# Performance work log

Hardware: AMD Instinct MI355X
Metric: run time of the kernel (lower is better)

## Reference

```python
import jax, jax.numpy as jnp
import numpy as np

EMBED_DIM = 512
NUM_HEADS = 16
WIN = (8, 8)
N_TOK = WIN[0] * WIN[1]           # 64 tokens per window
HEAD_DIM = EMBED_DIM // NUM_HEADS  # 32
SCALE = HEAD_DIM ** -0.5
B_WIN = 1024                       # batch * num_windows
NUM_WINDOWS = 256                  # windows per image -> batch images = 4


def _relative_bias_index(window_size):
    wh, ww = window_size
    coords = np.stack(np.meshgrid(np.arange(wh), np.arange(ww), indexing='ij'))  # (2, wh, ww)
    flat = coords.reshape(2, -1)                                   # (2, N)
    rel = (flat[:, :, None] - flat[:, None, :]).transpose(1, 2, 0)  # (N, N, 2)
    rel[:, :, 0] += wh - 1
    rel[:, :, 1] += ww - 1
    rel[:, :, 0] *= 2 * ww - 1
    return rel.sum(-1)  # (N, N) int


def setup_inputs() -> dict:
    key = jax.random.key(0)
    ks = jax.random.split(key, 6)
    x = jax.random.normal(ks[0], (B_WIN, N_TOK, EMBED_DIM), dtype=jnp.float32)
    attention_mask = jax.random.normal(ks[1], (NUM_WINDOWS, N_TOK, N_TOK), dtype=jnp.float32)
    qkv_w = jax.random.normal(ks[2], (EMBED_DIM, 3 * EMBED_DIM), dtype=jnp.float32) * 0.02
    qkv_b = jnp.zeros((3 * EMBED_DIM,), dtype=jnp.float32)
    proj_w = jax.random.normal(ks[3], (EMBED_DIM, EMBED_DIM), dtype=jnp.float32) * 0.02
    proj_b = jnp.zeros((EMBED_DIM,), dtype=jnp.float32)
    n_bias = (2 * WIN[0] - 1) * (2 * WIN[1] - 1)  # 225
    bias_table = jax.random.normal(ks[4], (n_bias, NUM_HEADS), dtype=jnp.float32) * 0.02
    rel_index = jnp.asarray(_relative_bias_index(WIN), dtype=jnp.int32)  # (N, N)
    return {"x": x, "attention_mask": attention_mask, "qkv_w": qkv_w, "qkv_b": qkv_b,
            "proj_w": proj_w, "proj_b": proj_b, "bias_table": bias_table, "rel_index": rel_index}


def reference(x, attention_mask, qkv_w, qkv_b, proj_w, proj_b, bias_table, rel_index):
    B, N, C = x.shape
    nw = attention_mask.shape[0]
    bimg = B // nw
    qkv = x @ qkv_w + qkv_b                              # (B, N, 3C)
    # original rearrange 'b n (h d c) -> d b n h c' groups last dim as (heads, 3, head_dim)
    qkv = qkv.reshape(B, N, NUM_HEADS, 3, HEAD_DIM)
    q, k, v = qkv[..., 0, :], qkv[..., 1, :], qkv[..., 2, :]  # each (B, N, H, hd)
    attn = jnp.einsum('bqhd,bkhd->bhqk', q, k) * SCALE        # (B, H, N, N)
    bias = bias_table[rel_index].transpose(2, 0, 1)           # (H, N, N)
    attn = attn + bias[None]
    attn = attn.reshape(bimg, nw, NUM_HEADS, N, N) + attention_mask[None, :, None]
    attn = jax.nn.softmax(attn, axis=-1).reshape(B, NUM_HEADS, N, N)
    out = jnp.einsum('bhqk,bkhd->bqhd', attn, v).reshape(B, N, C)
    return out @ proj_w + proj_b
```

## Files before the change

kernel.cpp:

```cpp
#include <hip/hip_runtime.h>
#include <hip/hip_bf16.h>


typedef unsigned short u16;
typedef __bf16 bx8 __attribute__((ext_vector_type(8)));
typedef float f4_t __attribute__((ext_vector_type(4)));

#define QKV_ELEMS 33554432ull
#define SCALE 0.17677669529663687f

static __device__ __forceinline__ u16 f2b(float f) {
    return __builtin_bit_cast(u16, (__bf16)f);
}

__global__ void wt_k(const float* __restrict__ W, u16* __restrict__ Wt,
                     int K, int N) {
    int idx = blockIdx.x * 256 + threadIdx.x;
    if (idx >= N * K) return;
    int n = idx / K, k = idx - n * K;
    Wt[idx] = f2b(W[(size_t)k * N + n]);
}

__global__ void bias_k(const float* __restrict__ bias_table,
                       const int* __restrict__ rel_index,
                       float* __restrict__ bias_full) {
    int idx = blockIdx.x * 256 + threadIdx.x;
    int h = idx >> 12, rc = idx & 4095;
    bias_full[idx] = bias_table[rel_index[rc] * 16 + h];
}

template <int MODE>
__global__ __launch_bounds__(256) void gemm_k(
    const void* __restrict__ Av, const u16* __restrict__ Bt,
    const float* __restrict__ bias, void* __restrict__ Out, int K) {
    const int tid  = threadIdx.x;
    const int wave = tid >> 6, lane = tid & 63;
    const int quad = lane >> 4, l16 = lane & 15;
    const int wm = wave >> 1, wn = wave & 1;
    const int m0 = blockIdx.y * 128, n0 = blockIdx.x * 128;
    const int N = gridDim.x * 128;

    __shared__ alignas(16) u16 a_s[128 * 40];
    __shared__ alignas(16) u16 b_s[128 * 40];

    f4_t acc[4][4];
#pragma unroll
    for (int i = 0; i < 4; ++i)
#pragma unroll
        for (int j = 0; j < 4; ++j) acc[i][j] = (f4_t){0.f, 0.f, 0.f, 0.f};

    for (int kt = 0; kt < K; kt += 32) {
        if (MODE == 0) {
            const float* A = (const float*)Av;
#pragma unroll
            for (int r = 0; r < 4; ++r) {
                int f = tid + 256 * r;
                int row = f >> 3, c4 = (f & 7) * 4;
                float4 v = *(const float4*)(A + (size_t)(m0 + row) * K + kt + c4);
                ushort4 p;
                p.x = f2b(v.x); p.y = f2b(v.y); p.z = f2b(v.z); p.w = f2b(v.w);
                *(ushort4*)&a_s[row * 40 + c4] = p;
            }
        } else {
            const u16* A = (const u16*)Av;
#pragma unroll
            for (int r = 0; r < 2; ++r) {
                int u = tid + 256 * r;
                int row = u >> 2, c8 = (u & 3) * 8;
                uint4 v = *(const uint4*)(A + (size_t)(m0 + row) * K + kt + c8);
                *(uint4*)&a_s[row * 40 + c8] = v;
            }
        }
#pragma unroll
        for (int r = 0; r < 2; ++r) {
            int u = tid + 256 * r;
            int row = u >> 2, c8 = (u & 3) * 8;
            uint4 v = *(const uint4*)(Bt + (size_t)(n0 + row) * K + kt + c8);
            *(uint4*)&b_s[row * 40 + c8] = v;
        }
        __syncthreads();

        bx8 af[4], bfr[4];
#pragma unroll
        for (int mt = 0; mt < 4; ++mt)
            af[mt] = *(const bx8*)&a_s[(wm * 64 + mt * 16 + l16) * 40 + quad * 8];
#pragma unroll
        for (int nt = 0; nt < 4; ++nt)
            bfr[nt] = *(const bx8*)&b_s[(wn * 64 + nt * 16 + l16) * 40 + quad * 8];
#pragma unroll
        for (int mt = 0; mt < 4; ++mt)
#pragma unroll
            for (int nt = 0; nt < 4; ++nt)
                acc[mt][nt] = __builtin_amdgcn_mfma_f32_16x16x32_bf16(
                    af[mt], bfr[nt], acc[mt][nt], 0, 0, 0);
        __syncthreads();
    }

    if (MODE == 0) {
        u16* qkv = (u16*)Out;
#pragma unroll
        for (int mt = 0; mt < 4; ++mt)
#pragma unroll
            for (int nt = 0; nt < 4; ++nt)
#pragma unroll
                for (int i = 0; i < 4; ++i) {
                    int r = m0 + wm * 64 + mt * 16 + quad * 4 + i;
                    int c = n0 + wn * 64 + nt * 16 + l16;
                    float v = acc[mt][nt][i] + bias[c];
                    int w = r >> 6, tok = r & 63;
                    int h = c / 96, rr = c - h * 96;
                    int which = rr >> 5, dd = rr & 31;
                    qkv[(size_t)which * QKV_ELEMS +
                        ((size_t)((w * 16 + h) * 64 + tok)) * 32 + dd] = f2b(v);
                }
    } else {
        float* Of = (float*)Out;
#pragma unroll
        for (int mt = 0; mt < 4; ++mt)
#pragma unroll
            for (int nt = 0; nt < 4; ++nt)
#pragma unroll
                for (int i = 0; i < 4; ++i) {
                    int r = m0 + wm * 64 + mt * 16 + quad * 4 + i;
                    int c = n0 + wn * 64 + nt * 16 + l16;
                    Of[(size_t)r * N + c] = acc[mt][nt][i] + bias[c];
                }
    }
}

__global__ __launch_bounds__(256) void attn_k(
    const u16* __restrict__ qkv, const float* __restrict__ mask,
    const float* __restrict__ biasf, u16* __restrict__ attn_out) {
    const int bx = blockIdx.x;
    const int w = bx >> 4, h = bx & 15;
    const int wmk = w & 255;
    const int tid = threadIdx.x;
    const int wave = tid >> 6, lane = tid & 63;
    const int quad = lane >> 4, l16 = lane & 15;

    __shared__ alignas(16) u16 q_s[64 * 40];
    __shared__ alignas(16) u16 k_s[64 * 40];
    __shared__ alignas(16) u16 vT[32 * 72];
    __shared__ float s_s[64 * 68];
    __shared__ alignas(16) u16 p_s[64 * 72];

    const size_t base = (size_t)((w << 4) + h) * 2048;
    {
        int tok = tid >> 2, d0 = (tid & 3) * 8;
        uint4 qv = *(const uint4*)(qkv + base + tid * 8);
        *(uint4*)&q_s[tok * 40 + d0] = qv;
        uint4 kv = *(const uint4*)(qkv + QKV_ELEMS + base + tid * 8);
        *(uint4*)&k_s[tok * 40 + d0] = kv;
        uint4 vv = *(const uint4*)(qkv + 2 * QKV_ELEMS + base + tid * 8);
        const u16* pv = (const u16*)&vv;
#pragma unroll
        for (int j = 0; j < 8; ++j) vT[(d0 + j) * 72 + tok] = pv[j];
    }
    __syncthreads();

    {
        bx8 a = *(const bx8*)&q_s[(wave * 16 + l16) * 40 + quad * 8];
#pragma unroll
        for (int nt = 0; nt < 4; ++nt) {
            bx8 b = *(const bx8*)&k_s[(nt * 16 + l16) * 40 + quad * 8];
            f4_t acc = (f4_t){0.f, 0.f, 0.f, 0.f};
            acc = __builtin_amdgcn_mfma_f32_16x16x32_bf16(a, b, acc, 0, 0, 0);
#pragma unroll
            for (int i = 0; i < 4; ++i) {
                int r = wave * 16 + quad * 4 + i;
                int c = nt * 16 + l16;
                float s = acc[i] * SCALE + biasf[(h << 12) + (r << 6) + c] +
                          mask[((size_t)wmk * 64 + r) * 64 + c];
                s_s[r * 68 + c] = s;
            }
        }
    }
    __syncthreads();

    {
        int row = tid >> 2, j = (tid & 3) * 16;
        float mx = -1e30f;
#pragma unroll
        for (int cc = 0; cc < 16; ++cc) mx = fmaxf(mx, s_s[row * 68 + j + cc]);
        mx = fmaxf(mx, __shfl_xor(mx, 1));
        mx = fmaxf(mx, __shfl_xor(mx, 2));
        float e[16], sum = 0.f;
#pragma unroll
        for (int cc = 0; cc < 16; ++cc) {
            e[cc] = __expf(s_s[row * 68 + j + cc] - mx);
            sum += e[cc];
        }
        sum += __shfl_xor(sum, 1);
        sum += __shfl_xor(sum, 2);
        float inv = 1.f / sum;
#pragma unroll
        for (int cc = 0; cc < 16; ++cc) p_s[row * 72 + j + cc] = f2b(e[cc] * inv);
    }
    __syncthreads();

    {
#pragma unroll
        for (int nt = 0; nt < 2; ++nt) {
            f4_t acc = (f4_t){0.f, 0.f, 0.f, 0.f};
#pragma unroll
            for (int ks = 0; ks < 2; ++ks) {
                bx8 a = *(const bx8*)&p_s[(wave * 16 + l16) * 72 + ks * 32 + quad * 8];
                bx8 b = *(const bx8*)&vT[(nt * 16 + l16) * 72 + ks * 32 + quad * 8];
                acc = __builtin_amdgcn_mfma_f32_16x16x32_bf16(a, b, acc, 0, 0, 0);
            }
#pragma unroll
            for (int i = 0; i < 4; ++i) {
                int r = wave * 16 + quad * 4 + i;
                int c = nt * 16 + l16;
                attn_out[((size_t)(w * 64 + r) << 9) + (h << 5) + c] = f2b(acc[i]);
            }
        }
    }
}

extern "C" void kernel_launch(void* const* d_in, const int* in_sizes, int n_in,
                              void* d_out, int out_size, void* d_ws,
                              size_t ws_size, hipStream_t stream) {
    const float* x      = (const float*)d_in[0];
    const float* mask   = (const float*)d_in[1];
    const float* qkv_w  = (const float*)d_in[2];
    const float* qkv_b  = (const float*)d_in[3];
    const float* proj_w = (const float*)d_in[4];
    const float* proj_b = (const float*)d_in[5];
    const float* bias_t = (const float*)d_in[6];
    const int*   rel    = (const int*)d_in[7];
    float* out = (float*)d_out;

    char* ws = (char*)d_ws;
    u16* Wt1 = (u16*)ws;      ws += (size_t)1536 * 512 * 2;
    u16* Wt2 = (u16*)ws;      ws += (size_t)512 * 512 * 2;
    float* biasf = (float*)ws; ws += (size_t)16 * 64 * 64 * 4;
    u16* qkv = (u16*)ws;      ws += 3 * QKV_ELEMS * 2;
    u16* attn = (u16*)ws;     ws += QKV_ELEMS * 2;

    wt_k<<<3072, 256, 0, stream>>>(qkv_w, Wt1, 512, 1536);
    wt_k<<<1024, 256, 0, stream>>>(proj_w, Wt2, 512, 512);
    bias_k<<<256, 256, 0, stream>>>(bias_t, rel, biasf);
    gemm_k<0><<<dim3(12, 512), 256, 0, stream>>>(x, Wt1, qkv_b, qkv, 512);
    attn_k<<<16384, 256, 0, stream>>>(qkv, mask, biasf, attn);
    gemm_k<1><<<dim3(4, 512), 256, 0, stream>>>(attn, Wt2, proj_b, out, 512);
}
```

Before: 580.0 us.

## Pre-convert x to bf16 and load GEMM tiles via global_load_lds

Adds a separate pass that converts x from fp32 to bf16, writing into the attn buffer, which is reused as scratch. Both GEMMs then take bf16 A and stage A and B tiles directly into LDS with the global_load_lds builtin, bypassing registers. The padded LDS stride of 40 becomes an unpadded 32. The aim is to cut register traffic and the per-tile fp32 conversion that was repeated for every N block. In exchange it adds an extra fp32 read and bf16 write of x, and the unpadded layout may raise LDS bank conflicts on the fragment reads.

```diff
diff --git a/kernel.cpp b/kernel.cpp
--- a/kernel.cpp
+++ b/kernel.cpp
@@ -11,6 +11,23 @@
 
 static __device__ __forceinline__ u16 f2b(float f) {
     return __builtin_bit_cast(u16, (__bf16)f);
+}
+
+typedef const unsigned int __attribute__((address_space(1)))* gas_t;
+typedef unsigned int __attribute__((address_space(3)))* las_t;
+static __device__ __forceinline__ void glds16(const void* g, void* l) {
+    __builtin_amdgcn_global_load_lds((gas_t)g, (las_t)l, 16, 0, 0);
+}
+
+__global__ void cvt_k(const float* __restrict__ X, u16* __restrict__ Xb) {
+    size_t i = ((size_t)blockIdx.x * 256 + threadIdx.x) * 8;
+    float4 v0 = *(const float4*)(X + i);
+    float4 v1 = *(const float4*)(X + i + 4);
+    ushort4 p0, p1;
+    p0.x = f2b(v0.x); p0.y = f2b(v0.y); p0.z = f2b(v0.z); p0.w = f2b(v0.w);
+    p1.x = f2b(v1.x); p1.y = f2b(v1.y); p1.z = f2b(v1.z); p1.w = f2b(v1.w);
+    *(ushort4*)(Xb + i) = p0;
+    *(ushort4*)(Xb + i + 4) = p1;
 }
 
 __global__ void wt_k(const float* __restrict__ W, u16* __restrict__ Wt,
@@ -31,7 +48,7 @@
 
 template <int MODE>
 __global__ __launch_bounds__(256) void gemm_k(
-    const void* __restrict__ Av, const u16* __restrict__ Bt,
+    const u16* __restrict__ A, const u16* __restrict__ Bt,
     const float* __restrict__ bias, void* __restrict__ Out, int K) {
     const int tid  = threadIdx.x;
     const int wave = tid >> 6, lane = tid & 63;
@@ -40,8 +57,11 @@
     const int m0 = blockIdx.y * 128, n0 = blockIdx.x * 128;
     const int N = gridDim.x * 128;
 
-    __shared__ alignas(16) u16 a_s[128 * 40];
-    __shared__ alignas(16) u16 b_s[128 * 40];
+    __shared__ alignas(16) u16 a_s[128 * 32];
+    __shared__ alignas(16) u16 b_s[128 * 32];
+
+    const int lr = lane >> 2, lc = (lane & 3) * 8;
+    const int w16 = wave * 16;
 
     f4_t acc[4][4];
 #pragma unroll
@@ -50,43 +70,21 @@
         for (int j = 0; j < 4; ++j) acc[i][j] = (f4_t){0.f, 0.f, 0.f, 0.f};
 
     for (int kt = 0; kt < K; kt += 32) {
-        if (MODE == 0) {
-            const float* A = (const float*)Av;
-#pragma unroll
-            for (int r = 0; r < 4; ++r) {
-                int f = tid + 256 * r;
-                int row = f >> 3, c4 = (f & 7) * 4;
-                float4 v = *(const float4*)(A + (size_t)(m0 + row) * K + kt + c4);
-                ushort4 p;
-                p.x = f2b(v.x); p.y = f2b(v.y); p.z = f2b(v.z); p.w = f2b(v.w);
-                *(ushort4*)&a_s[row * 40 + c4] = p;
-            }
-        } else {
-            const u16* A = (const u16*)Av;
-#pragma unroll
-            for (int r = 0; r < 2; ++r) {
-                int u = tid + 256 * r;
-                int row = u >> 2, c8 = (u & 3) * 8;
-                uint4 v = *(const uint4*)(A + (size_t)(m0 + row) * K + kt + c8);
-                *(uint4*)&a_s[row * 40 + c8] = v;
-            }
-        }
-#pragma unroll
-        for (int r = 0; r < 2; ++r) {
-            int u = tid + 256 * r;
-            int row = u >> 2, c8 = (u & 3) * 8;
-            uint4 v = *(const uint4*)(Bt + (size_t)(n0 + row) * K + kt + c8);
-            *(uint4*)&b_s[row * 40 + c8] = v;
-        }
+        const u16* Ab = A + (size_t)m0 * K + kt;
+        const u16* Bb = Bt + (size_t)n0 * K + kt;
+        glds16(Ab + (size_t)(w16 + lr) * K + lc,      &a_s[w16 * 32]);
+        glds16(Ab + (size_t)(w16 + 64 + lr) * K + lc, &a_s[(w16 + 64) * 32]);
+        glds16(Bb + (size_t)(w16 + lr) * K + lc,      &b_s[w16 * 32]);
+        glds16(Bb + (size_t)(w16 + 64 + lr) * K + lc, &b_s[(w16 + 64) * 32]);
         __syncthreads();
 
         bx8 af[4], bfr[4];
 #pragma unroll
         for (int mt = 0; mt < 4; ++mt)
-            af[mt] = *(const bx8*)&a_s[(wm * 64 + mt * 16 + l16) * 40 + quad * 8];
+            af[mt] = *(const bx8*)&a_s[(wm * 64 + mt * 16 + l16) * 32 + quad * 8];
 #pragma unroll
         for (int nt = 0; nt < 4; ++nt)
-            bfr[nt] = *(const bx8*)&b_s[(wn * 64 + nt * 16 + l16) * 40 + quad * 8];
+            bfr[nt] = *(const bx8*)&b_s[(wn * 64 + nt * 16 + l16) * 32 + quad * 8];
 #pragma unroll
         for (int mt = 0; mt < 4; ++mt)
 #pragma unroll
@@ -237,11 +235,13 @@
     float* biasf = (float*)ws; ws += (size_t)16 * 64 * 64 * 4;
     u16* qkv = (u16*)ws;      ws += 3 * QKV_ELEMS * 2;
     u16* attn = (u16*)ws;     ws += QKV_ELEMS * 2;
-
+    u16* xb = attn;
+
+    cvt_k<<<16384, 256, 0, stream>>>(x, xb);
     wt_k<<<3072, 256, 0, stream>>>(qkv_w, Wt1, 512, 1536);
     wt_k<<<1024, 256, 0, stream>>>(proj_w, Wt2, 512, 512);
     bias_k<<<256, 256, 0, stream>>>(bias_t, rel, biasf);
-    gemm_k<0><<<dim3(12, 512), 256, 0, stream>>>(x, Wt1, qkv_b, qkv, 512);
+    gemm_k<0><<<dim3(12, 512), 256, 0, stream>>>(xb, Wt1, qkv_b, qkv, 512);
     attn_k<<<16384, 256, 0, stream>>>(qkv, mask, biasf, attn);
     gemm_k<1><<<dim3(4, 512), 256, 0, stream>>>(attn, Wt2, proj_b, out, 512);
 }
```

Result: no change. 572.1 us (-1.4%).
